# Kernel optimization log

Hardware: AMD Instinct MI355X
Metric: run time of the kernel (lower is better)

## Reference

```python
import jax, jax.numpy as jnp
import numpy as np

N_LABELS = 16
LABEL_DIM = 128
BN_EPS = 1e-5


def setup_inputs() -> dict:
    key = jax.random.key(0)
    k1, k2 = jax.random.split(key, 2)
    B, T, D = 8, 512, 768
    return {
        "features": jax.random.normal(k1, (B, T, D), dtype=jnp.float32),
        "mask": jnp.ones((B, T), dtype=bool),
        "bn_gamma": jnp.ones((D,), dtype=jnp.float32),
        "bn_beta": jnp.zeros((D,), dtype=jnp.float32),
        "ff_w": jax.random.normal(k2, (LABEL_DIM * N_LABELS * 2, D), dtype=jnp.float32) * 0.02,
        "ff_b": jnp.zeros((LABEL_DIM * N_LABELS * 2,), dtype=jnp.float32),
        "label_bias": jnp.zeros((N_LABELS,), dtype=jnp.float32),
    }


def reference(features, mask, bn_gamma, bn_beta, ff_w, ff_b, label_bias):
    B, T, D = features.shape
    m = mask.astype(features.dtype)[..., None]  # [B,T,1]
    denom = jnp.maximum(m.sum(), 1.0)
    # FlatBatchNorm (training mode): stats over masked tokens, zeros elsewhere
    mean = (features * m).sum(axis=(0, 1)) / denom
    var = (((features - mean) ** 2) * m).sum(axis=(0, 1)) / denom
    normed = (features - mean) * jax.lax.rsqrt(var + BN_EPS) * bn_gamma + bn_beta
    feats = normed * m  # res[mask]=flat, zeros elsewhere
    # FFN + relu -> [B,T,n_labels,label_dim,2]
    h = jax.nn.relu(jnp.einsum('btd,od->bto', feats, ff_w) + ff_b)
    h = h.reshape(B, T, N_LABELS, LABEL_DIM, 2)
    start_f = h[..., 0]  # [B,T,L,D]
    end_f = h[..., 1]
    # biaffine span scores: [B, L, T_start, T_end]
    scores = jnp.einsum('bsld,beld->blse', start_f, end_f) + label_bias[None, :, None, None]
    triu = jnp.triu(jnp.ones((T, T), dtype=bool))
    spans_mask = triu[None, None] & mask[:, None, :, None] & mask[:, None, None, :]  # [B,L,T,T] via broadcast
    spans_mask = jnp.broadcast_to(spans_mask, scores.shape)
    return scores, spans_mask
```

## Files before the change

### kernel.cpp

```cpp
#include <hip/hip_runtime.h>

#define B_    8
#define T_    512
#define D_    768
#define L_    16
#define DL_   128
#define NO_   4096
#define M_    4096
#define BN_EPS 1e-5f

typedef __attribute__((ext_vector_type(8))) short short8;
typedef __attribute__((ext_vector_type(4))) float f32x4;

__device__ inline unsigned short f2bf(float x) {
    unsigned int u = __float_as_uint(x);
    unsigned int r = (u + 0x7fffu + ((u >> 16) & 1u)) >> 16;
    return (unsigned short)r;
}

__global__ void k_stats(const float* __restrict__ f, const int* __restrict__ mask,
                        float* __restrict__ stats) {
    int tid = threadIdx.x;
    int t0  = blockIdx.x * 64;
    float s0 = 0.f, s1 = 0.f, s2 = 0.f, q0 = 0.f, q1 = 0.f, q2 = 0.f;
    for (int tt = 0; tt < 64; ++tt) {
        int t = t0 + tt;
        float m = mask[t] ? 1.f : 0.f;
        const float* row = f + (size_t)t * D_;
        float x0 = row[tid];
        float x1 = row[tid + 256];
        float x2 = row[tid + 512];
        s0 += x0 * m; q0 += x0 * x0 * m;
        s1 += x1 * m; q1 += x1 * x1 * m;
        s2 += x2 * m; q2 += x2 * x2 * m;
    }
    atomicAdd(&stats[tid      ], s0);
    atomicAdd(&stats[tid + 256], s1);
    atomicAdd(&stats[tid + 512], s2);
    atomicAdd(&stats[768 + tid      ], q0);
    atomicAdd(&stats[768 + tid + 256], q1);
    atomicAdd(&stats[768 + tid + 512], q2);
    if (tid == 0) {
        int c = 0;
        for (int tt = 0; tt < 64; ++tt) c += (mask[t0 + tt] ? 1 : 0);
        atomicAdd(&stats[1536], (float)c);
    }
}

__global__ void k_finalize(const float* __restrict__ gamma, const float* __restrict__ beta,
                           float* __restrict__ stats) {
    int d = threadIdx.x;
    float denom = fmaxf(stats[1536], 1.f);
    float mean  = stats[d] / denom;
    float var   = fmaxf(stats[768 + d] / denom - mean * mean, 0.f);
    float sc    = gamma[d] * rsqrtf(var + BN_EPS);
    stats[2048 + d] = sc;
    stats[2816 + d] = beta[d] - mean * sc;
}

__global__ void k_norm(const float4* __restrict__ f4, const int* __restrict__ mask,
                       const float* __restrict__ stats, unsigned short* __restrict__ outp) {
    int i  = blockIdx.x * 256 + threadIdx.x;
    int d4 = i % (D_ / 4);
    int t  = i / (D_ / 4);
    float m = mask[t] ? 1.f : 0.f;
    float4 v = f4[i];
    int d = d4 * 4;
    float r0 = (v.x * stats[2048 + d + 0] + stats[2816 + d + 0]) * m;
    float r1 = (v.y * stats[2048 + d + 1] + stats[2816 + d + 1]) * m;
    float r2 = (v.z * stats[2048 + d + 2] + stats[2816 + d + 2]) * m;
    float r3 = (v.w * stats[2048 + d + 3] + stats[2816 + d + 3]) * m;
    ushort4 o;
    o.x = f2bf(r0); o.y = f2bf(r1); o.z = f2bf(r2); o.w = f2bf(r3);
    ((ushort4*)outp)[i] = o;
}

__global__ void k_castw(const float4* __restrict__ w4, unsigned short* __restrict__ outp) {
    int i = blockIdx.x * 256 + threadIdx.x;
    float4 v = w4[i];
    ushort4 o;
    o.x = f2bf(v.x); o.y = f2bf(v.y); o.z = f2bf(v.z); o.w = f2bf(v.w);
    ((ushort4*)outp)[i] = o;
}

__launch_bounds__(256)
__global__ void k_ffn(const unsigned short* __restrict__ A, const unsigned short* __restrict__ W,
                      const float* __restrict__ bias,
                      unsigned short* __restrict__ startp, unsigned short* __restrict__ endp) {
    __shared__ alignas(16) unsigned short As[128][40];
    __shared__ alignas(16) unsigned short Bs[128][40];
    int tid  = threadIdx.x;
    int bm   = blockIdx.x, bn = blockIdx.y;
    int wave = tid >> 6, lane = tid & 63;
    int wm = wave >> 1, wn = wave & 1;
    int lr = lane & 15, quad = lane >> 4;
    f32x4 acc[4][4] = {};
    const int K = D_;
    for (int k0 = 0; k0 < K; k0 += 32) {
#pragma unroll
        for (int p = 0; p < 2; ++p) {
            int c   = tid + p * 256;
            int row = c >> 2, seg = c & 3;
            uint4 va = *(const uint4*)(A + ((size_t)(bm * 128 + row) * K + k0 + seg * 8));
            *(uint4*)&As[row][seg * 8] = va;
            uint4 vb = *(const uint4*)(W + ((size_t)(bn * 128 + row) * K + k0 + seg * 8));
            *(uint4*)&Bs[row][seg * 8] = vb;
        }
        __syncthreads();
        short8 a[4], b[4];
#pragma unroll
        for (int i = 0; i < 4; ++i) a[i] = *(const short8*)&As[wm * 64 + i * 16 + lr][quad * 8];
#pragma unroll
        for (int i = 0; i < 4; ++i) b[i] = *(const short8*)&Bs[wn * 64 + i * 16 + lr][quad * 8];
#pragma unroll
        for (int i = 0; i < 4; ++i)
#pragma unroll
            for (int j = 0; j < 4; ++j)
                acc[i][j] = __builtin_amdgcn_mfma_f32_16x16x32_bf16(a[i], b[j], acc[i][j], 0, 0, 0);
        __syncthreads();
    }
#pragma unroll
    for (int i = 0; i < 4; ++i) {
#pragma unroll
        for (int j = 0; j < 4; ++j) {
            int col  = bn * 128 + wn * 64 + j * 16 + lr;
            int l    = col >> 8;
            int dd   = (col >> 1) & 127;
            int cbit = col & 1;
            unsigned short* dst = cbit ? endp : startp;
            float bv = bias[col];
#pragma unroll
            for (int r = 0; r < 4; ++r) {
                int row = bm * 128 + wm * 64 + i * 16 + quad * 4 + r;
                float v = acc[i][j][r] + bv;
                v = fmaxf(v, 0.f);
                int bb = row >> 9, tt = row & 511;
                dst[(((size_t)(bb * 16 + l) * 512 + tt) << 7) + dd] = f2bf(v);
            }
        }
    }
}

__launch_bounds__(256)
__global__ void k_biaffine(const unsigned short* __restrict__ startp,
                           const unsigned short* __restrict__ endp,
                           const float* __restrict__ lbias, float* __restrict__ out) {
    __shared__ alignas(16) unsigned short As[128][40];
    __shared__ alignas(16) unsigned short Bs[128][40];
    int tid = threadIdx.x;
    int bm = blockIdx.x, bn = blockIdx.y;
    int bl = blockIdx.z;
    const unsigned short* A  = startp + (size_t)bl * 512 * 128;
    const unsigned short* Bp = endp   + (size_t)bl * 512 * 128;
    int wave = tid >> 6, lane = tid & 63;
    int wm = wave >> 1, wn = wave & 1;
    int lr = lane & 15, quad = lane >> 4;
    f32x4 acc[4][4] = {};
    const int K = DL_;
    for (int k0 = 0; k0 < K; k0 += 32) {
#pragma unroll
        for (int p = 0; p < 2; ++p) {
            int c   = tid + p * 256;
            int row = c >> 2, seg = c & 3;
            uint4 va = *(const uint4*)(A  + ((size_t)(bm * 128 + row) * K + k0 + seg * 8));
            *(uint4*)&As[row][seg * 8] = va;
            uint4 vb = *(const uint4*)(Bp + ((size_t)(bn * 128 + row) * K + k0 + seg * 8));
            *(uint4*)&Bs[row][seg * 8] = vb;
        }
        __syncthreads();
        short8 a[4], b[4];
#pragma unroll
        for (int i = 0; i < 4; ++i) a[i] = *(const short8*)&As[wm * 64 + i * 16 + lr][quad * 8];
#pragma unroll
        for (int i = 0; i < 4; ++i) b[i] = *(const short8*)&Bs[wn * 64 + i * 16 + lr][quad * 8];
#pragma unroll
        for (int i = 0; i < 4; ++i)
#pragma unroll
            for (int j = 0; j < 4; ++j)
                acc[i][j] = __builtin_amdgcn_mfma_f32_16x16x32_bf16(a[i], b[j], acc[i][j], 0, 0, 0);
        __syncthreads();
    }
    float lb = lbias[bl & 15];
    float* obase = out + (size_t)bl * 512 * 512;
#pragma unroll
    for (int i = 0; i < 4; ++i) {
#pragma unroll
        for (int j = 0; j < 4; ++j) {
            int e = bn * 128 + wn * 64 + j * 16 + lr;
#pragma unroll
            for (int r = 0; r < 4; ++r) {
                int s = bm * 128 + wm * 64 + i * 16 + quad * 4 + r;
                obase[(size_t)s * 512 + e] = acc[i][j][r] + lb;
            }
        }
    }
}

__global__ void k_mask(const int* __restrict__ mask, float* __restrict__ out1) {
    int idx = blockIdx.x * 256 + threadIdx.x;
    int e4 = idx & 127;
    int s  = (idx >> 7) & 511;
    int b  = idx >> 16;
    int e0 = e4 * 4;
    float ms = mask[b * 512 + s] ? 1.f : 0.f;
    float4 v;
    v.x = (s <= e0 + 0 && mask[b * 512 + e0 + 0]) ? ms : 0.f;
    v.y = (s <= e0 + 1 && mask[b * 512 + e0 + 1]) ? ms : 0.f;
    v.z = (s <= e0 + 2 && mask[b * 512 + e0 + 2]) ? ms : 0.f;
    v.w = (s <= e0 + 3 && mask[b * 512 + e0 + 3]) ? ms : 0.f;
#pragma unroll
    for (int l = 0; l < 16; ++l) {
        ((float4*)out1)[((size_t)((b * 16 + l) * 512 + s) * 512 + e0) >> 2] = v;
    }
}

extern "C" void kernel_launch(void* const* d_in, const int* in_sizes, int n_in,
                              void* d_out, int out_size, void* d_ws, size_t ws_size,
                              hipStream_t stream) {
    const float* features = (const float*)d_in[0];
    const int*   mask     = (const int*)d_in[1];
    const float* gamma    = (const float*)d_in[2];
    const float* beta     = (const float*)d_in[3];
    const float* ffw      = (const float*)d_in[4];
    const float* ffb      = (const float*)d_in[5];
    const float* lbias    = (const float*)d_in[6];

    float* out_scores = (float*)d_out;
    float* out_mask   = out_scores + (size_t)B_ * L_ * T_ * T_;

    char* ws = (char*)d_ws;
    float*          stats  = (float*)ws;
    unsigned short* feats  = (unsigned short*)(ws + 16384);
    unsigned short* wbf    = (unsigned short*)(ws + 16384 + 6291456);
    unsigned short* startp = (unsigned short*)(ws + 12599296);
    unsigned short* endp   = (unsigned short*)(ws + 29376512);

    hipMemsetAsync(ws, 0, 16384, stream);
    k_stats<<<64, 256, 0, stream>>>(features, mask, stats);
    k_finalize<<<1, 768, 0, stream>>>(gamma, beta, stats);
    k_norm<<<3072, 256, 0, stream>>>((const float4*)features, mask, stats, feats);
    k_castw<<<3072, 256, 0, stream>>>((const float4*)ffw, wbf);
    dim3 g1(32, 32);
    k_ffn<<<g1, 256, 0, stream>>>(feats, wbf, ffb, startp, endp);
    dim3 g2(4, 4, 128);
    k_biaffine<<<g2, 256, 0, stream>>>(startp, endp, lbias, out_scores);
    k_mask<<<2048, 256, 0, stream>>>(mask, out_mask);
}
```

Before: 375.4 us.

## Fuse mask into biaffine, merge prep kernels, async LDS loads, permute weights

The span-mask kernel is folded into the biaffine epilogue, so each output tile writes its scores and mask together and one launch plus a separate pass over the output disappears. The norm and weight-cast kernels are merged into one launch. The weight rows are permuted during the cast so each FFN column tile maps to one label and one start/end half, which simplifies the epilogue. Both GEMMs now fill shared memory with global_load_lds direct-to-LDS loads into unpadded tiles, and k_stats runs 256 blocks instead of 64 to use more CUs. Unpadded LDS tiles risk bank conflicts, and the fused mask writes lengthen the biaffine epilogue.

```diff
diff --git a/kernel.cpp b/kernel.cpp
--- a/kernel.cpp
+++ b/kernel.cpp
@@ -5,7 +5,6 @@
 #define D_    768
 #define L_    16
 #define DL_   128
-#define NO_   4096
 #define M_    4096
 #define BN_EPS 1e-5f
 
@@ -14,16 +13,21 @@
 
 __device__ inline unsigned short f2bf(float x) {
     unsigned int u = __float_as_uint(x);
-    unsigned int r = (u + 0x7fffu + ((u >> 16) & 1u)) >> 16;
-    return (unsigned short)r;
+    return (unsigned short)((u + 0x7fffu + ((u >> 16) & 1u)) >> 16);
+}
+
+__device__ inline void async16(const unsigned short* gptr, unsigned short* lptr) {
+    __builtin_amdgcn_global_load_lds(
+        (const __attribute__((address_space(1))) void*)gptr,
+        (__attribute__((address_space(3))) void*)lptr, 16, 0, 0);
 }
 
 __global__ void k_stats(const float* __restrict__ f, const int* __restrict__ mask,
                         float* __restrict__ stats) {
     int tid = threadIdx.x;
-    int t0  = blockIdx.x * 64;
+    int t0  = blockIdx.x * 16;
     float s0 = 0.f, s1 = 0.f, s2 = 0.f, q0 = 0.f, q1 = 0.f, q2 = 0.f;
-    for (int tt = 0; tt < 64; ++tt) {
+    for (int tt = 0; tt < 16; ++tt) {
         int t = t0 + tt;
         float m = mask[t] ? 1.f : 0.f;
         const float* row = f + (size_t)t * D_;
@@ -42,7 +46,7 @@
     atomicAdd(&stats[768 + tid + 512], q2);
     if (tid == 0) {
         int c = 0;
-        for (int tt = 0; tt < 64; ++tt) c += (mask[t0 + tt] ? 1 : 0);
+        for (int tt = 0; tt < 16; ++tt) c += (mask[t0 + tt] ? 1 : 0);
         atomicAdd(&stats[1536], (float)c);
     }
 }
@@ -58,60 +62,63 @@
     stats[2816 + d] = beta[d] - mean * sc;
 }
 
-__global__ void k_norm(const float4* __restrict__ f4, const int* __restrict__ mask,
-                       const float* __restrict__ stats, unsigned short* __restrict__ outp) {
-    int i  = blockIdx.x * 256 + threadIdx.x;
-    int d4 = i % (D_ / 4);
-    int t  = i / (D_ / 4);
-    float m = mask[t] ? 1.f : 0.f;
-    float4 v = f4[i];
-    int d = d4 * 4;
-    float r0 = (v.x * stats[2048 + d + 0] + stats[2816 + d + 0]) * m;
-    float r1 = (v.y * stats[2048 + d + 1] + stats[2816 + d + 1]) * m;
-    float r2 = (v.z * stats[2048 + d + 2] + stats[2816 + d + 2]) * m;
-    float r3 = (v.w * stats[2048 + d + 3] + stats[2816 + d + 3]) * m;
-    ushort4 o;
-    o.x = f2bf(r0); o.y = f2bf(r1); o.z = f2bf(r2); o.w = f2bf(r3);
-    ((ushort4*)outp)[i] = o;
-}
-
-__global__ void k_castw(const float4* __restrict__ w4, unsigned short* __restrict__ outp) {
-    int i = blockIdx.x * 256 + threadIdx.x;
-    float4 v = w4[i];
-    ushort4 o;
-    o.x = f2bf(v.x); o.y = f2bf(v.y); o.z = f2bf(v.z); o.w = f2bf(v.w);
-    ((ushort4*)outp)[i] = o;
+__global__ void k_prep(const float4* __restrict__ f4, const int* __restrict__ mask,
+                       const float* __restrict__ stats, unsigned short* __restrict__ feats,
+                       const float4* __restrict__ w4, unsigned short* __restrict__ wbf) {
+    int bx = blockIdx.x;
+    if (bx < 3072) {
+        int i  = bx * 256 + threadIdx.x;
+        int d4 = i % (D_ / 4);
+        int t  = i / (D_ / 4);
+        float m = mask[t] ? 1.f : 0.f;
+        float4 v = f4[i];
+        int d = d4 * 4;
+        ushort4 o;
+        o.x = f2bf((v.x * stats[2048 + d + 0] + stats[2816 + d + 0]) * m);
+        o.y = f2bf((v.y * stats[2048 + d + 1] + stats[2816 + d + 1]) * m);
+        o.z = f2bf((v.z * stats[2048 + d + 2] + stats[2816 + d + 2]) * m);
+        o.w = f2bf((v.w * stats[2048 + d + 3] + stats[2816 + d + 3]) * m);
+        ((ushort4*)feats)[i] = o;
+    } else {
+        int i  = (bx - 3072) * 256 + threadIdx.x;
+        int o  = i / 192, cg = i % 192;
+        int nr = (o & 1) * 2048 + (o >> 8) * 128 + ((o >> 1) & 127);
+        float4 v = w4[i];
+        ushort4 u;
+        u.x = f2bf(v.x); u.y = f2bf(v.y); u.z = f2bf(v.z); u.w = f2bf(v.w);
+        ((ushort4*)wbf)[nr * 192 + cg] = u;
+    }
 }
 
 __launch_bounds__(256)
 __global__ void k_ffn(const unsigned short* __restrict__ A, const unsigned short* __restrict__ W,
-                      const float* __restrict__ bias,
+                      const float* __restrict__ ffb,
                       unsigned short* __restrict__ startp, unsigned short* __restrict__ endp) {
-    __shared__ alignas(16) unsigned short As[128][40];
-    __shared__ alignas(16) unsigned short Bs[128][40];
+    __shared__ alignas(16) unsigned short As[128 * 32];
+    __shared__ alignas(16) unsigned short Bs[128 * 32];
     int tid  = threadIdx.x;
     int bm   = blockIdx.x, bn = blockIdx.y;
     int wave = tid >> 6, lane = tid & 63;
     int wm = wave >> 1, wn = wave & 1;
     int lr = lane & 15, quad = lane >> 4;
+    int srow = lane >> 2, sseg = (lane & 3) * 8;
     f32x4 acc[4][4] = {};
     const int K = D_;
+    const unsigned short* Abase = A + (size_t)(bm * 128) * K;
+    const unsigned short* Wbase = W + (size_t)(bn * 128) * K;
     for (int k0 = 0; k0 < K; k0 += 32) {
 #pragma unroll
         for (int p = 0; p < 2; ++p) {
-            int c   = tid + p * 256;
-            int row = c >> 2, seg = c & 3;
-            uint4 va = *(const uint4*)(A + ((size_t)(bm * 128 + row) * K + k0 + seg * 8));
-            *(uint4*)&As[row][seg * 8] = va;
-            uint4 vb = *(const uint4*)(W + ((size_t)(bn * 128 + row) * K + k0 + seg * 8));
-            *(uint4*)&Bs[row][seg * 8] = vb;
+            int r0 = (wave * 2 + p) * 16;
+            async16(Abase + (size_t)(r0 + srow) * K + k0 + sseg, &As[r0 * 32]);
+            async16(Wbase + (size_t)(r0 + srow) * K + k0 + sseg, &Bs[r0 * 32]);
         }
         __syncthreads();
         short8 a[4], b[4];
 #pragma unroll
-        for (int i = 0; i < 4; ++i) a[i] = *(const short8*)&As[wm * 64 + i * 16 + lr][quad * 8];
-#pragma unroll
-        for (int i = 0; i < 4; ++i) b[i] = *(const short8*)&Bs[wn * 64 + i * 16 + lr][quad * 8];
+        for (int i = 0; i < 4; ++i) a[i] = *(const short8*)&As[(wm * 64 + i * 16 + lr) * 32 + quad * 8];
+#pragma unroll
+        for (int i = 0; i < 4; ++i) b[i] = *(const short8*)&Bs[(wn * 64 + i * 16 + lr) * 32 + quad * 8];
 #pragma unroll
         for (int i = 0; i < 4; ++i)
 #pragma unroll
@@ -119,23 +126,20 @@
                 acc[i][j] = __builtin_amdgcn_mfma_f32_16x16x32_bf16(a[i], b[j], acc[i][j], 0, 0, 0);
         __syncthreads();
     }
-#pragma unroll
-    for (int i = 0; i < 4; ++i) {
-#pragma unroll
-        for (int j = 0; j < 4; ++j) {
-            int col  = bn * 128 + wn * 64 + j * 16 + lr;
-            int l    = col >> 8;
-            int dd   = (col >> 1) & 127;
-            int cbit = col & 1;
-            unsigned short* dst = cbit ? endp : startp;
-            float bv = bias[col];
+    int c = bn >> 4, l = bn & 15;
+    unsigned short* dstb = c ? endp : startp;
+#pragma unroll
+    for (int j = 0; j < 4; ++j) {
+        int dd = wn * 64 + j * 16 + lr;
+        float bv = ffb[l * 256 + dd * 2 + c];
+#pragma unroll
+        for (int i = 0; i < 4; ++i) {
 #pragma unroll
             for (int r = 0; r < 4; ++r) {
                 int row = bm * 128 + wm * 64 + i * 16 + quad * 4 + r;
-                float v = acc[i][j][r] + bv;
-                v = fmaxf(v, 0.f);
                 int bb = row >> 9, tt = row & 511;
-                dst[(((size_t)(bb * 16 + l) * 512 + tt) << 7) + dd] = f2bf(v);
+                float v = fmaxf(acc[i][j][r] + bv, 0.f);
+                dstb[(((size_t)(bb * 16 + l) * 512 + tt) << 7) + dd] = f2bf(v);
             }
         }
     }
@@ -144,73 +148,57 @@
 __launch_bounds__(256)
 __global__ void k_biaffine(const unsigned short* __restrict__ startp,
                            const unsigned short* __restrict__ endp,
-                           const float* __restrict__ lbias, float* __restrict__ out) {
-    __shared__ alignas(16) unsigned short As[128][40];
-    __shared__ alignas(16) unsigned short Bs[128][40];
+                           const float* __restrict__ lbias, const int* __restrict__ mask,
+                           float* __restrict__ outs, float* __restrict__ outm) {
+    __shared__ alignas(16) unsigned short As[128 * 32];
+    __shared__ alignas(16) unsigned short Bs[128 * 32];
     int tid = threadIdx.x;
     int bm = blockIdx.x, bn = blockIdx.y;
     int bl = blockIdx.z;
-    const unsigned short* A  = startp + (size_t)bl * 512 * 128;
-    const unsigned short* Bp = endp   + (size_t)bl * 512 * 128;
+    int b  = bl >> 4;
+    const unsigned short* Abase = startp + ((size_t)bl * 512 + bm * 128) * 128;
+    const unsigned short* Bbase = endp   + ((size_t)bl * 512 + bn * 128) * 128;
     int wave = tid >> 6, lane = tid & 63;
     int wm = wave >> 1, wn = wave & 1;
     int lr = lane & 15, quad = lane >> 4;
+    int srow = lane >> 2, sseg = (lane & 3) * 8;
     f32x4 acc[4][4] = {};
-    const int K = DL_;
-    for (int k0 = 0; k0 < K; k0 += 32) {
+    for (int k0 = 0; k0 < 128; k0 += 32) {
 #pragma unroll
         for (int p = 0; p < 2; ++p) {
-            int c   = tid + p * 256;
-            int row = c >> 2, seg = c & 3;
-            uint4 va = *(const uint4*)(A  + ((size_t)(bm * 128 + row) * K + k0 + seg * 8));
-            *(uint4*)&As[row][seg * 8] = va;
-            uint4 vb = *(const uint4*)(Bp + ((size_t)(bn * 128 + row) * K + k0 + seg * 8));
-            *(uint4*)&Bs[row][seg * 8] = vb;
-        }
-        __syncthreads();
-        short8 a[4], b[4];
-#pragma unroll
-        for (int i = 0; i < 4; ++i) a[i] = *(const short8*)&As[wm * 64 + i * 16 + lr][quad * 8];
-#pragma unroll
-        for (int i = 0; i < 4; ++i) b[i] = *(const short8*)&Bs[wn * 64 + i * 16 + lr][quad * 8];
+            int r0 = (wave * 2 + p) * 16;
+            async16(Abase + (size_t)(r0 + srow) * 128 + k0 + sseg, &As[r0 * 32]);
+            async16(Bbase + (size_t)(r0 + srow) * 128 + k0 + sseg, &Bs[r0 * 32]);
+        }
+        __syncthreads();
+        short8 a[4], b8[4];
+#pragma unroll
+        for (int i = 0; i < 4; ++i) a[i]  = *(const short8*)&As[(wm * 64 + i * 16 + lr) * 32 + quad * 8];
+#pragma unroll
+        for (int i = 0; i < 4; ++i) b8[i] = *(const short8*)&Bs[(wn * 64 + i * 16 + lr) * 32 + quad * 8];
 #pragma unroll
         for (int i = 0; i < 4; ++i)
 #pragma unroll
             for (int j = 0; j < 4; ++j)
-                acc[i][j] = __builtin_amdgcn_mfma_f32_16x16x32_bf16(a[i], b[j], acc[i][j], 0, 0, 0);
+                acc[i][j] = __builtin_amdgcn_mfma_f32_16x16x32_bf16(a[i], b8[j], acc[i][j], 0, 0, 0);
         __syncthreads();
     }
     float lb = lbias[bl & 15];
-    float* obase = out + (size_t)bl * 512 * 512;
+    float* os = outs + (size_t)bl * 262144;
+    float* om = outm + (size_t)bl * 262144;
 #pragma unroll
     for (int i = 0; i < 4; ++i) {
 #pragma unroll
-        for (int j = 0; j < 4; ++j) {
-            int e = bn * 128 + wn * 64 + j * 16 + lr;
-#pragma unroll
-            for (int r = 0; r < 4; ++r) {
-                int s = bm * 128 + wm * 64 + i * 16 + quad * 4 + r;
-                obase[(size_t)s * 512 + e] = acc[i][j][r] + lb;
+        for (int r = 0; r < 4; ++r) {
+            int s = bm * 128 + wm * 64 + i * 16 + quad * 4 + r;
+            float msv = mask[b * 512 + s] ? 1.f : 0.f;
+#pragma unroll
+            for (int j = 0; j < 4; ++j) {
+                int e = bn * 128 + wn * 64 + j * 16 + lr;
+                os[(size_t)s * 512 + e] = acc[i][j][r] + lb;
+                om[(size_t)s * 512 + e] = (s <= e && mask[b * 512 + e]) ? msv : 0.f;
             }
         }
-    }
-}
-
-__global__ void k_mask(const int* __restrict__ mask, float* __restrict__ out1) {
-    int idx = blockIdx.x * 256 + threadIdx.x;
-    int e4 = idx & 127;
-    int s  = (idx >> 7) & 511;
-    int b  = idx >> 16;
-    int e0 = e4 * 4;
-    float ms = mask[b * 512 + s] ? 1.f : 0.f;
-    float4 v;
-    v.x = (s <= e0 + 0 && mask[b * 512 + e0 + 0]) ? ms : 0.f;
-    v.y = (s <= e0 + 1 && mask[b * 512 + e0 + 1]) ? ms : 0.f;
-    v.z = (s <= e0 + 2 && mask[b * 512 + e0 + 2]) ? ms : 0.f;
-    v.w = (s <= e0 + 3 && mask[b * 512 + e0 + 3]) ? ms : 0.f;
-#pragma unroll
-    for (int l = 0; l < 16; ++l) {
-        ((float4*)out1)[((size_t)((b * 16 + l) * 512 + s) * 512 + e0) >> 2] = v;
     }
 }
 
@@ -236,13 +224,12 @@
     unsigned short* endp   = (unsigned short*)(ws + 29376512);
 
     hipMemsetAsync(ws, 0, 16384, stream);
-    k_stats<<<64, 256, 0, stream>>>(features, mask, stats);
+    k_stats<<<256, 256, 0, stream>>>(features, mask, stats);
     k_finalize<<<1, 768, 0, stream>>>(gamma, beta, stats);
-    k_norm<<<3072, 256, 0, stream>>>((const float4*)features, mask, stats, feats);
-    k_castw<<<3072, 256, 0, stream>>>((const float4*)ffw, wbf);
+    k_prep<<<6144, 256, 0, stream>>>((const float4*)features, mask, stats, feats,
+                                     (const float4*)ffw, wbf);
     dim3 g1(32, 32);
     k_ffn<<<g1, 256, 0, stream>>>(feats, wbf, ffb, startp, endp);
     dim3 g2(4, 4, 128);
-    k_biaffine<<<g2, 256, 0, stream>>>(startp, endp, lbias, out_scores);
-    k_mask<<<2048, 256, 0, stream>>>(mask, out_mask);
-}
+    k_biaffine<<<g2, 256, 0, stream>>>(startp, endp, lbias, mask, out_scores, out_mask);
+}
```

After: 382.2 us. Within noise of the previous version (+1.8%).
